# Optimization experiments

Hardware: AMD Instinct MI355X
Metric: run time of the kernel (lower is better)

The kernel has to match this reference:

```python
import jax, jax.numpy as jnp
import numpy as np

EMBED_DIM = 1024
NUM_HEADS = 16
DEPTH = EMBED_DIM // NUM_HEADS
SCALE_FACTOR = 0.5
SEQ = 2048
BATCH = 2


def setup_inputs() -> dict:
    key = jax.random.key(0)
    ks = jax.random.split(key, 6)
    x = jax.random.normal(ks[0], (SEQ, BATCH, EMBED_DIM), dtype=jnp.float32)
    attn_mask = jnp.zeros((SEQ, SEQ), dtype=jnp.float32)
    key_padding_mask = jnp.zeros((BATCH, SEQ), dtype=bool)
    # Linear params (torch convention: y = x @ W.T + b)
    s_in = 1.0 / np.sqrt(EMBED_DIM)
    qkv_w = jax.random.uniform(ks[1], (3 * EMBED_DIM, EMBED_DIM), jnp.float32, -s_in, s_in)
    qkv_b = jax.random.uniform(ks[2], (3 * EMBED_DIM,), jnp.float32, -s_in, s_in)
    out_w = jax.random.uniform(ks[3], (EMBED_DIM, EMBED_DIM), jnp.float32, -s_in, s_in)
    out_b = jax.random.uniform(ks[4], (EMBED_DIM,), jnp.float32, -s_in, s_in)
    return {"x": x, "attn_mask": attn_mask, "key_padding_mask": key_padding_mask,
            "qkv_w": qkv_w, "qkv_b": qkv_b, "out_w": out_w, "out_b": out_b}


def reference(x, attn_mask, key_padding_mask, qkv_w, qkv_b, out_w, out_b):
    # x: [S, B, E] -> [B, S, E]
    xb = jnp.transpose(x, (1, 0, 2))
    B, S, E = xb.shape
    qkv = xb @ qkv_w.T + qkv_b                       # [B, S, 3E]
    q, k, v = jnp.split(qkv, 3, axis=2)
    def split_heads(t):                              # [B, S, E] -> [B, H, S, d]
        return jnp.transpose(t.reshape(B, S, NUM_HEADS, DEPTH), (0, 2, 1, 3))
    q, k, v = split_heads(q), split_heads(k), split_heads(v)
    scores = jnp.einsum('bhqd,bhkd->bhqk', q, k) / (DEPTH ** SCALE_FACTOR)
    scores = jnp.where(key_padding_mask[:, None, None, :], -jnp.inf, scores)
    scores = scores + attn_mask[None, None, :, :]
    attn = jax.nn.softmax(scores, axis=-1)           # [B, H, S, S] (dropout p=0)
    wa = jnp.einsum('bhqk,bhkd->bhqd', attn, v)      # [B, H, S, d]
    wa = jnp.transpose(wa, (0, 2, 1, 3)).reshape(B, S, E)
    out = wa @ out_w.T + out_b                       # [B, S, E]
    out = jnp.transpose(out, (1, 0, 2))              # [S, B, E]
    attn_mean = jnp.mean(attn, axis=1)               # [B, S, S]
    return out, attn_mean
```

## Files before the change

kernel.cpp:

```cpp
#include <hip/hip_runtime.h>
#include <hip/hip_bf16.h>


#define Sq 2048
#define Bb 2
#define Ee 1024
#define Hh 16
#define Dd 64
#define LOG2E 1.4426950408889634f
#define QSCALE 0.18033688011112042f

typedef __attribute__((ext_vector_type(8))) short bhalf8;
typedef __attribute__((ext_vector_type(4))) float f32x4;

__device__ __forceinline__ void gld16(const __hip_bfloat16* g, __hip_bfloat16* l) {
    __builtin_amdgcn_global_load_lds(
        (const __attribute__((address_space(1))) unsigned int*)g,
        (__attribute__((address_space(3))) unsigned int*)l, 16, 0, 0);
}

__device__ __forceinline__ int pkbf(float a, float b) {
    union { __hip_bfloat16 h[2]; int i; } u;
    u.h[0] = __float2bfloat16(a);
    u.h[1] = __float2bfloat16(b);
    return u.i;
}

__device__ __forceinline__ int tile_off(int s) {
    return ((s >> 2) & 1) * 2048 + (s >> 7) * 512 + (s & 3) * 128 + ((s >> 3) & 15) * 8;
}

__device__ __forceinline__ int kperm(int p) {
    return (p & 3) | (((p >> 5) & 1) << 2) | ((p & 12) << 1) | (((p >> 4) & 1) << 5);
}

__global__ __launch_bounds__(256) void prep_k(
    const float* __restrict__ x, const float* __restrict__ am,
    const unsigned int* __restrict__ kpm32,
    const float* __restrict__ qkv_w, const float* __restrict__ out_w,
    __hip_bfloat16* __restrict__ xb, __hip_bfloat16* __restrict__ qwb,
    __hip_bfloat16* __restrict__ owb, unsigned int* __restrict__ flag)
{
    const long i = (long)blockIdx.x*256 + threadIdx.x;
    if (i < 1048576) {
        float4 v = ((const float4*)am)[i];
        bool nz = (v.x != 0.f) | (v.y != 0.f) | (v.z != 0.f) | (v.w != 0.f);
        if (i < 1024) nz |= (kpm32[i] != 0u);
        if (__ballot(nz)) { if ((threadIdx.x & 63) == 0) atomicOr(flag, 1u); }
    } else if (i < 2097152) {
        const long j = i - 1048576;
        const int m = (int)(j >> 8), e4 = (int)(j & 255);
        const int b = m >> 11, s = m & 2047;
        float4 v = ((const float4*)x)[(size_t)(s*Bb + b)*256 + e4];
        union { __hip_bfloat16 h[4]; uint2 u; } o;
        o.h[0]=__float2bfloat16(v.x); o.h[1]=__float2bfloat16(v.y);
        o.h[2]=__float2bfloat16(v.z); o.h[3]=__float2bfloat16(v.w);
        ((uint2*)xb)[(size_t)m*256 + e4] = o.u;
    } else if (i < 2883584) {
        const long j = i - 2097152;
        float4 v = ((const float4*)qkv_w)[j];
        union { __hip_bfloat16 h[4]; uint2 u; } o;
        o.h[0]=__float2bfloat16(v.x); o.h[1]=__float2bfloat16(v.y);
        o.h[2]=__float2bfloat16(v.z); o.h[3]=__float2bfloat16(v.w);
        ((uint2*)qwb)[j] = o.u;
    } else if (i < 3145728) {
        const long j = i - 2883584;
        float4 v = ((const float4*)out_w)[j];
        union { __hip_bfloat16 h[4]; uint2 u; } o;
        o.h[0]=__float2bfloat16(v.x); o.h[1]=__float2bfloat16(v.y);
        o.h[2]=__float2bfloat16(v.z); o.h[3]=__float2bfloat16(v.w);
        ((uint2*)owb)[j] = o.u;
    }
}

__global__ __launch_bounds__(256) void gemm_qkv(
    const __hip_bfloat16* __restrict__ A, const __hip_bfloat16* __restrict__ Bw,
    const float* __restrict__ bias,
    __hip_bfloat16* __restrict__ Qp, __hip_bfloat16* __restrict__ Kp,
    __hip_bfloat16* __restrict__ Vt)
{
    __shared__ __align__(16) __hip_bfloat16 As[128*32];
    __shared__ __align__(16) __hip_bfloat16 Bs[128*32];
    const int t = threadIdx.x;
    const int l = t & 63, lm = l & 15, quad = l >> 4;
    const int w = t >> 6;
    const int mw = (w & 1)*64, nw = (w >> 1)*64;
    const int m0 = blockIdx.y*128, n0 = blockIdx.x*128;

    const int srow = t >> 2;
    const int scol = (t & 3)*8;
    const __hip_bfloat16* ag = A  + (size_t)(m0 + srow)*1024 + scol;
    const __hip_bfloat16* bg = Bw + (size_t)(n0 + srow)*1024 + scol;
    __hip_bfloat16* al = As + t*8;
    __hip_bfloat16* bl = Bs + t*8;

    f32x4 acc[4][4] = {};
    for (int k0 = 0; k0 < 1024; k0 += 32) {
        __syncthreads();
        gld16(ag + k0, al);
        gld16(ag + (size_t)64*1024 + k0, al + 2048);
        gld16(bg + k0, bl);
        gld16(bg + (size_t)64*1024 + k0, bl + 2048);
        __syncthreads();
        bhalf8 af[4], bf[4];
#pragma unroll
        for (int i = 0; i < 4; i++) {
            af[i] = *(const bhalf8*)&As[(mw + i*16 + lm)*32 + quad*8];
            bf[i] = *(const bhalf8*)&Bs[(nw + i*16 + lm)*32 + quad*8];
        }
#pragma unroll
        for (int mf = 0; mf < 4; mf++)
#pragma unroll
            for (int nf = 0; nf < 4; nf++)
                acc[mf][nf] = __builtin_amdgcn_mfma_f32_16x16x32_bf16(af[mf], bf[nf], acc[mf][nf], 0,0,0);
    }
#pragma unroll
    for (int nf = 0; nf < 4; nf++) {
        const int n = n0 + nw + nf*16 + lm;
        const float bz = bias[n];
        const int which = n >> 10, hh = (n >> 6) & 15, dd = n & 63;
#pragma unroll
        for (int mf = 0; mf < 4; mf++)
#pragma unroll
            for (int r = 0; r < 4; r++) {
                const int m = m0 + mw + mf*16 + quad*4 + r;
                const int b2 = m >> 11, s2 = m & 2047;
                const float vf = acc[mf][nf][r] + bz;
                if (which == 0)
                    Qp[((size_t)(b2*Hh + hh)*Sq + s2)*Dd + dd] = __float2bfloat16(vf * QSCALE);
                else if (which == 1)
                    Kp[((size_t)(b2*Hh + hh)*Sq + s2)*Dd + dd] = __float2bfloat16(vf);
                else
                    Vt[((size_t)(b2*Hh + hh)*Dd + dd)*Sq + s2] = __float2bfloat16(vf);
            }
    }
}

__global__ __launch_bounds__(256, 4) void attn_mfma(
    const __hip_bfloat16* __restrict__ Qp, const __hip_bfloat16* __restrict__ Kp,
    const __hip_bfloat16* __restrict__ Vt,
    const float* __restrict__ am, const unsigned char* __restrict__ kpm,
    const unsigned int* __restrict__ flag,
    __hip_bfloat16* __restrict__ wa, float* __restrict__ rlbuf)
{
    __shared__ __align__(16) __hip_bfloat16 Ks[4096];
    __shared__ __align__(16) __hip_bfloat16 Vs[4096];
    const int t = threadIdx.x;
    const int w = t >> 6, l = t & 63, lm = l & 15, quad = l >> 4;
    const int blk = blockIdx.x;
    const int xcd = blk & 7;
    const int qt  = (blk >> 3) & 31;
    const int grp = blk >> 8;
    const int bh  = grp*8 + xcd;
    const int b   = bh >> 4, h = bh & 15;
    const int q   = qt*64 + w*16 + lm;
    const bool masked = (flag[0] != 0u);

    const __hip_bfloat16* qbase = Qp + (size_t)bh*Sq*Dd;
    const __hip_bfloat16* kbase = Kp + (size_t)bh*Sq*Dd;
    const __hip_bfloat16* vbase = Vt + (size_t)bh*Dd*Sq;

    bhalf8 bq[2];
    bq[0] = *(const bhalf8*)(qbase + (size_t)q*Dd + quad*8);
    bq[1] = *(const bhalf8*)(qbase + (size_t)q*Dd + quad*8 + 32);

    f32x4 o[4] = {};
    float lsum = 0.f;

    const int off0 = tile_off(t), off1 = tile_off(t + 256);
    const int krow0 = kperm(t >> 3);
    const int krow1 = kperm(32 + (t >> 3));
    const int kcol  = (t & 7)*8;

    uint4 kreg0 = *(const uint4*)(kbase + (size_t)krow0*Dd + kcol);
    uint4 kreg1 = *(const uint4*)(kbase + (size_t)krow1*Dd + kcol);
    uint4 vreg0 = *(const uint4*)(vbase + (size_t)(t >> 3)*Sq + (t & 7)*8);
    uint4 vreg1 = *(const uint4*)(vbase + (size_t)((t + 256) >> 3)*Sq + (t & 7)*8);

    for (int kt = 0; kt < 32; kt++) {
        __syncthreads();
        *(uint4*)&Ks[off0] = kreg0;
        *(uint4*)&Ks[off1] = kreg1;
        *(uint4*)&Vs[off0] = vreg0;
        *(uint4*)&Vs[off1] = vreg1;
        if (kt < 31) {
            const int kn = (kt + 1)*64;
            kreg0 = *(const uint4*)(kbase + (size_t)(kn + krow0)*Dd + kcol);
            kreg1 = *(const uint4*)(kbase + (size_t)(kn + krow1)*Dd + kcol);
            vreg0 = *(const uint4*)(vbase + (size_t)(t >> 3)*Sq + kn + (t & 7)*8);
            vreg1 = *(const uint4*)(vbase + (size_t)((t + 256) >> 3)*Sq + kn + (t & 7)*8);
        }
        __syncthreads();

        const int k0 = kt*64;
        f32x4 s[4] = {};
#pragma unroll
        for (int f = 0; f < 2; f++) {
            bhalf8 ak[4];
#pragma unroll
            for (int j = 0; j < 4; j++)
                ak[j] = *(const bhalf8*)&Ks[f*2048 + j*512 + l*8];
#pragma unroll
            for (int j = 0; j < 4; j++)
                s[j] = __builtin_amdgcn_mfma_f32_16x16x32_bf16(ak[j], bq[f], s[j], 0,0,0);
        }

        int pk[4][2];
#pragma unroll
        for (int j = 0; j < 4; j++) {
            float p[4];
#pragma unroll
            for (int r = 0; r < 4; r++) {
                float sv = s[j][r];
                if (masked) {
                    const int key = k0 + 32*(j & 1) + 8*quad + 4*(j >> 1) + r;
                    const float km = kpm[b*Sq + key] ? -1e30f : 0.0f;
                    sv += (am[(size_t)q*Sq + key] + km) * LOG2E;
                }
                p[r] = exp2f(sv);
            }
            lsum += (p[0]+p[1]) + (p[2]+p[3]);
            pk[j][0] = pkbf(p[0], p[1]);
            pk[j][1] = pkbf(p[2], p[3]);
        }

#pragma unroll
        for (int ks = 0; ks < 2; ks++) {
            union { int i[4]; bhalf8 v; } bp;
            bp.i[0] = pk[ks][0];
            bp.i[1] = pk[ks][1];
            bp.i[2] = pk[ks + 2][0];
            bp.i[3] = pk[ks + 2][1];
            bhalf8 av[4];
#pragma unroll
            for (int nd = 0; nd < 4; nd++)
                av[nd] = *(const bhalf8*)&Vs[ks*2048 + nd*512 + l*8];
#pragma unroll
            for (int nd = 0; nd < 4; nd++)
                o[nd] = __builtin_amdgcn_mfma_f32_16x16x32_bf16(av[nd], bp.v, o[nd], 0,0,0);
        }
    }

    lsum += __shfl_xor(lsum, 16, 64);
    lsum += __shfl_xor(lsum, 32, 64);
    const float rl = 1.0f / lsum;
    if (quad == 0) rlbuf[(size_t)bh*Sq + q] = rl;

#pragma unroll
    for (int nd = 0; nd < 4; nd++) {
        union { __hip_bfloat16 hx[4]; uint2 u; } ou;
#pragma unroll
        for (int r = 0; r < 4; r++) ou.hx[r] = __float2bfloat16(o[nd][r] * rl);
        *(uint2*)(wa + ((size_t)b*Sq + q)*Ee + h*Dd + nd*16 + quad*4) = ou.u;
    }
}

__global__ __launch_bounds__(256, 4) void attn_mean_k(
    const __hip_bfloat16* __restrict__ Qp, const __hip_bfloat16* __restrict__ Kp,
    const float* __restrict__ am, const unsigned char* __restrict__ kpm,
    const unsigned int* __restrict__ flag,
    const float* __restrict__ rlbuf, float* __restrict__ attn_mean)
{
    __shared__ __align__(16) __hip_bfloat16 Ks[4096];
    __shared__ __align__(16) __hip_bfloat16 Qs[8192];
    const int t = threadIdx.x;
    const int w = t >> 6, l = t & 63, lm = l & 15, quad = l >> 4;
    const int b  = blockIdx.z;
    const int q0 = blockIdx.y * 128;
    const int kc = blockIdx.x * 64;
    const int q0w = q0 + w*32;
    const bool masked = (flag[0] != 0u);

    const int koff = tile_off(t);
    const int koff1 = tile_off(t + 256);
    int qoff[4];
#pragma unroll
    for (int i = 0; i < 4; i++) {
        const int s = t + i*256;
        qoff[i] = (s >> 8)*2048 + ((s >> 7) & 1)*1024 + ((s >> 2) & 1)*512
                + (s & 3)*128 + ((s >> 3) & 15)*8;
    }

    float macc[2][4][4] = {};

    const __hip_bfloat16* kb0 = Kp + ((size_t)(b*Hh)*Sq + kc)*Dd;
    const __hip_bfloat16* qb0 = Qp + ((size_t)(b*Hh)*Sq + q0)*Dd;
    uint4 kr0 = *(const uint4*)(kb0 + (size_t)t*8);
    uint4 kr1 = *(const uint4*)(kb0 + (size_t)(t + 256)*8);
    uint4 qr[4];
#pragma unroll
    for (int i = 0; i < 4; i++) qr[i] = *(const uint4*)(qb0 + (size_t)(t + i*256)*8);

    for (int h = 0; h < Hh; h++) {
        __syncthreads();
        *(uint4*)&Ks[koff]  = kr0;
        *(uint4*)&Ks[koff1] = kr1;
#pragma unroll
        for (int i = 0; i < 4; i++) *(uint4*)&Qs[qoff[i]] = qr[i];
        if (h < Hh-1) {
            const __hip_bfloat16* kbn = Kp + ((size_t)(b*Hh + h+1)*Sq + kc)*Dd;
            const __hip_bfloat16* qbn = Qp + ((size_t)(b*Hh + h+1)*Sq + q0)*Dd;
            kr0 = *(const uint4*)(kbn + (size_t)t*8);
            kr1 = *(const uint4*)(kbn + (size_t)(t + 256)*8);
#pragma unroll
            for (int i = 0; i < 4; i++) qr[i] = *(const uint4*)(qbn + (size_t)(t + i*256)*8);
        }
        __syncthreads();

        const int bh = b*Hh + h;
        bhalf8 bk[8];
#pragma unroll
        for (int f = 0; f < 2; f++)
#pragma unroll
            for (int j = 0; j < 4; j++)
                bk[f*4+j] = *(const bhalf8*)&Ks[f*2048 + j*512 + l*8];

#pragma unroll
        for (int su = 0; su < 2; su++) {
            f32x4 s[4] = {};
#pragma unroll
            for (int f = 0; f < 2; f++) {
                bhalf8 aq = *(const bhalf8*)&Qs[w*2048 + su*1024 + f*512 + l*8];
#pragma unroll
                for (int j = 0; j < 4; j++)
                    s[j] = __builtin_amdgcn_mfma_f32_16x16x32_bf16(aq, bk[f*4+j], s[j], 0,0,0);
            }
            float rl4[4];
#pragma unroll
            for (int r = 0; r < 4; r++)
                rl4[r] = rlbuf[(size_t)bh*Sq + q0w + su*16 + quad*4 + r] * 0.0625f;
#pragma unroll
            for (int j = 0; j < 4; j++)
#pragma unroll
                for (int r = 0; r < 4; r++) {
                    float sv = s[j][r];
                    if (masked) {
                        const int key = kc + j*16 + lm;
                        const float km = kpm[b*Sq + key] ? -1e30f : 0.0f;
                        sv += (am[(size_t)(q0w + su*16 + quad*4 + r)*Sq + key] + km) * LOG2E;
                    }
                    macc[su][j][r] += exp2f(sv) * rl4[r];
                }
        }
    }
#pragma unroll
    for (int su = 0; su < 2; su++)
#pragma unroll
        for (int j = 0; j < 4; j++)
#pragma unroll
            for (int r = 0; r < 4; r++)
                attn_mean[((size_t)b*Sq + q0w + su*16 + quad*4 + r)*Sq + kc + j*16 + lm] =
                    macc[su][j][r];
}

__global__ __launch_bounds__(256) void gemm_out(
    const __hip_bfloat16* __restrict__ A, const __hip_bfloat16* __restrict__ Bw,
    const float* __restrict__ bias, float* __restrict__ outp)
{
    __shared__ __align__(16) __hip_bfloat16 As[128*32];
    __shared__ __align__(16) __hip_bfloat16 Bs[128*32];
    const int t = threadIdx.x;
    const int l = t & 63, lm = l & 15, quad = l >> 4;
    const int w = t >> 6;
    const int mw = (w & 1)*64, nw = (w >> 1)*64;
    const int m0 = blockIdx.y*128, n0 = blockIdx.x*128;

    const int srow = t >> 2;
    const int scol = (t & 3)*8;
    const __hip_bfloat16* ag = A  + (size_t)(m0 + srow)*1024 + scol;
    const __hip_bfloat16* bg = Bw + (size_t)(n0 + srow)*1024 + scol;
    __hip_bfloat16* al = As + t*8;
    __hip_bfloat16* bl = Bs + t*8;

    f32x4 acc[4][4] = {};
    for (int k0 = 0; k0 < 1024; k0 += 32) {
        __syncthreads();
        gld16(ag + k0, al);
        gld16(ag + (size_t)64*1024 + k0, al + 2048);
        gld16(bg + k0, bl);
        gld16(bg + (size_t)64*1024 + k0, bl + 2048);
        __syncthreads();
        bhalf8 af[4], bf[4];
#pragma unroll
        for (int i = 0; i < 4; i++) {
            af[i] = *(const bhalf8*)&As[(mw + i*16 + lm)*32 + quad*8];
            bf[i] = *(const bhalf8*)&Bs[(nw + i*16 + lm)*32 + quad*8];
        }
#pragma unroll
        for (int mf = 0; mf < 4; mf++)
#pragma unroll
            for (int nf = 0; nf < 4; nf++)
                acc[mf][nf] = __builtin_amdgcn_mfma_f32_16x16x32_bf16(af[mf], bf[nf], acc[mf][nf], 0,0,0);
    }
#pragma unroll
    for (int nf = 0; nf < 4; nf++) {
        const int n = n0 + nw + nf*16 + lm;
        const float bz = bias[n];
#pragma unroll
        for (int mf = 0; mf < 4; mf++)
#pragma unroll
            for (int r = 0; r < 4; r++) {
                const int m = m0 + mw + mf*16 + quad*4 + r;
                const int b2 = m >> 11, s2 = m & 2047;
                outp[((size_t)s2*Bb + b2)*Ee + n] = acc[mf][nf][r] + bz;
            }
    }
}

extern "C" void kernel_launch(void* const* d_in, const int* in_sizes, int n_in,
                              void* d_out, int out_size, void* d_ws, size_t ws_size,
                              hipStream_t stream) {
    const float*         x         = (const float*)d_in[0];
    const float*         attn_mask = (const float*)d_in[1];
    const unsigned char* kpm       = (const unsigned char*)d_in[2];
    const float*         qkv_w     = (const float*)d_in[3];
    const float*         qkv_b     = (const float*)d_in[4];
    const float*         out_w     = (const float*)d_in[5];
    const float*         out_b     = (const float*)d_in[6];

    float* outp      = (float*)d_out;
    float* attn_mean = outp + 4194304;

    __hip_bfloat16* xb  = (__hip_bfloat16*)d_ws;
    __hip_bfloat16* qwb = xb  + 4194304;
    __hip_bfloat16* owb = qwb + 3145728;
    __hip_bfloat16* Qp  = owb + 1048576;
    __hip_bfloat16* Kp  = Qp  + 4194304;
    __hip_bfloat16* Vt  = Kp  + 4194304;
    __hip_bfloat16* wab = Vt  + 4194304;
    float* rlbuf        = (float*)(wab + 4194304);
    unsigned int* flag  = (unsigned int*)(rlbuf + 65536);

    hipMemsetAsync(flag, 0, sizeof(unsigned int), stream);
    prep_k<<<12288, 256, 0, stream>>>(x, attn_mask, (const unsigned int*)kpm,
                                      qkv_w, out_w, xb, qwb, owb, flag);
    gemm_qkv<<<dim3(24, 32), 256, 0, stream>>>(xb, qwb, qkv_b, Qp, Kp, Vt);
    attn_mfma<<<dim3(1024), 256, 0, stream>>>(Qp, Kp, Vt, attn_mask, kpm, flag, wab, rlbuf);
    attn_mean_k<<<dim3(32, 16, Bb), 256, 0, stream>>>(Qp, Kp, attn_mask, kpm, flag, rlbuf, attn_mean);
    gemm_out<<<dim3(8, 32), 256, 0, stream>>>(wab, owb, out_b, outp);
}
```

Measured before the change: 370.2 us.

## Halve attn_mean query tile and load Q/K via direct global-to-LDS copies

The attention-mean kernel now handles 64 queries per block instead of 128, doubling the grid to 2048 blocks and halving the Q shared-memory tile. The register-staged prefetch of the next head's Q/K tiles is replaced by global_load_lds direct copies issued each head iteration. K fragments are now read from LDS inside the MFMA loop instead of being cached in registers. The goal is higher occupancy and less register pressure, at the cost of losing explicit prefetch overlap and re-reading each K tile for twice as many query blocks.

```diff
diff --git a/kernel.cpp b/kernel.cpp
--- a/kernel.cpp
+++ b/kernel.cpp
@@ -262,95 +262,61 @@
     const float* __restrict__ rlbuf, float* __restrict__ attn_mean)
 {
     __shared__ __align__(16) __hip_bfloat16 Ks[4096];
-    __shared__ __align__(16) __hip_bfloat16 Qs[8192];
+    __shared__ __align__(16) __hip_bfloat16 Qs[4096];
     const int t = threadIdx.x;
     const int w = t >> 6, l = t & 63, lm = l & 15, quad = l >> 4;
     const int b  = blockIdx.z;
-    const int q0 = blockIdx.y * 128;
+    const int q0 = blockIdx.y * 64;
     const int kc = blockIdx.x * 64;
-    const int q0w = q0 + w*32;
     const bool masked = (flag[0] != 0u);
 
-    const int koff = tile_off(t);
-    const int koff1 = tile_off(t + 256);
-    int qoff[4];
-#pragma unroll
-    for (int i = 0; i < 4; i++) {
-        const int s = t + i*256;
-        qoff[i] = (s >> 8)*2048 + ((s >> 7) & 1)*1024 + ((s >> 2) & 1)*512
-                + (s & 3)*128 + ((s >> 3) & 15)*8;
-    }
-
-    float macc[2][4][4] = {};
-
-    const __hip_bfloat16* kb0 = Kp + ((size_t)(b*Hh)*Sq + kc)*Dd;
-    const __hip_bfloat16* qb0 = Qp + ((size_t)(b*Hh)*Sq + q0)*Dd;
-    uint4 kr0 = *(const uint4*)(kb0 + (size_t)t*8);
-    uint4 kr1 = *(const uint4*)(kb0 + (size_t)(t + 256)*8);
-    uint4 qr[4];
-#pragma unroll
-    for (int i = 0; i < 4; i++) qr[i] = *(const uint4*)(qb0 + (size_t)(t + i*256)*8);
+    const int s0 = ((w & 1) << 8) | (lm << 3) | ((w >> 1) << 2) | (l >> 4);
+    __hip_bfloat16* kl = Ks + w*1024;
+    __hip_bfloat16* ql = Qs + w*1024;
+
+    float macc[4][4] = {};
+    const float* rlp = rlbuf + (size_t)(b*Hh)*Sq + q0 + w*16 + quad*4;
 
     for (int h = 0; h < Hh; h++) {
-        __syncthreads();
-        *(uint4*)&Ks[koff]  = kr0;
-        *(uint4*)&Ks[koff1] = kr1;
-#pragma unroll
-        for (int i = 0; i < 4; i++) *(uint4*)&Qs[qoff[i]] = qr[i];
-        if (h < Hh-1) {
-            const __hip_bfloat16* kbn = Kp + ((size_t)(b*Hh + h+1)*Sq + kc)*Dd;
-            const __hip_bfloat16* qbn = Qp + ((size_t)(b*Hh + h+1)*Sq + q0)*Dd;
-            kr0 = *(const uint4*)(kbn + (size_t)t*8);
-            kr1 = *(const uint4*)(kbn + (size_t)(t + 256)*8);
-#pragma unroll
-            for (int i = 0; i < 4; i++) qr[i] = *(const uint4*)(qbn + (size_t)(t + i*256)*8);
-        }
-        __syncthreads();
-
-        const int bh = b*Hh + h;
-        bhalf8 bk[8];
-#pragma unroll
-        for (int f = 0; f < 2; f++)
-#pragma unroll
-            for (int j = 0; j < 4; j++)
-                bk[f*4+j] = *(const bhalf8*)&Ks[f*2048 + j*512 + l*8];
-
-#pragma unroll
-        for (int su = 0; su < 2; su++) {
-            f32x4 s[4] = {};
-#pragma unroll
-            for (int f = 0; f < 2; f++) {
-                bhalf8 aq = *(const bhalf8*)&Qs[w*2048 + su*1024 + f*512 + l*8];
-#pragma unroll
-                for (int j = 0; j < 4; j++)
-                    s[j] = __builtin_amdgcn_mfma_f32_16x16x32_bf16(aq, bk[f*4+j], s[j], 0,0,0);
+        const __hip_bfloat16* kg = Kp + ((size_t)(b*Hh + h)*Sq + kc)*Dd + s0*8;
+        const __hip_bfloat16* qg = Qp + ((size_t)(b*Hh + h)*Sq + q0)*Dd + s0*8;
+        __syncthreads();
+        gld16(kg, kl);       gld16(kg + 1024, kl + 512);
+        gld16(qg, ql);       gld16(qg + 1024, ql + 512);
+        __syncthreads();
+
+        f32x4 s[4] = {};
+#pragma unroll
+        for (int f = 0; f < 2; f++) {
+            bhalf8 aq = *(const bhalf8*)&Qs[f*2048 + w*512 + l*8];
+#pragma unroll
+            for (int j = 0; j < 4; j++) {
+                bhalf8 bk = *(const bhalf8*)&Ks[f*2048 + j*512 + l*8];
+                s[j] = __builtin_amdgcn_mfma_f32_16x16x32_bf16(aq, bk, s[j], 0,0,0);
             }
-            float rl4[4];
-#pragma unroll
-            for (int r = 0; r < 4; r++)
-                rl4[r] = rlbuf[(size_t)bh*Sq + q0w + su*16 + quad*4 + r] * 0.0625f;
-#pragma unroll
-            for (int j = 0; j < 4; j++)
-#pragma unroll
-                for (int r = 0; r < 4; r++) {
-                    float sv = s[j][r];
-                    if (masked) {
-                        const int key = kc + j*16 + lm;
-                        const float km = kpm[b*Sq + key] ? -1e30f : 0.0f;
-                        sv += (am[(size_t)(q0w + su*16 + quad*4 + r)*Sq + key] + km) * LOG2E;
-                    }
-                    macc[su][j][r] += exp2f(sv) * rl4[r];
+        }
+        float rl4[4];
+#pragma unroll
+        for (int r = 0; r < 4; r++) rl4[r] = rlp[(size_t)h*Sq + r] * 0.0625f;
+#pragma unroll
+        for (int j = 0; j < 4; j++)
+#pragma unroll
+            for (int r = 0; r < 4; r++) {
+                float sv = s[j][r];
+                if (masked) {
+                    const int key = kc + j*16 + lm;
+                    const float km = kpm[b*Sq + key] ? -1e30f : 0.0f;
+                    sv += (am[(size_t)(q0 + w*16 + quad*4 + r)*Sq + key] + km) * LOG2E;
                 }
-        }
-    }
-#pragma unroll
-    for (int su = 0; su < 2; su++)
-#pragma unroll
-        for (int j = 0; j < 4; j++)
-#pragma unroll
-            for (int r = 0; r < 4; r++)
-                attn_mean[((size_t)b*Sq + q0w + su*16 + quad*4 + r)*Sq + kc + j*16 + lm] =
-                    macc[su][j][r];
+                macc[j][r] += exp2f(sv) * rl4[r];
+            }
+    }
+#pragma unroll
+    for (int j = 0; j < 4; j++)
+#pragma unroll
+        for (int r = 0; r < 4; r++)
+            attn_mean[((size_t)b*Sq + q0 + w*16 + quad*4 + r)*Sq + kc + j*16 + lm] =
+                macc[j][r];
 }
 
 __global__ __launch_bounds__(256) void gemm_out(
@@ -436,6 +402,6 @@
                                       qkv_w, out_w, xb, qwb, owb, flag);
     gemm_qkv<<<dim3(24, 32), 256, 0, stream>>>(xb, qwb, qkv_b, Qp, Kp, Vt);
     attn_mfma<<<dim3(1024), 256, 0, stream>>>(Qp, Kp, Vt, attn_mask, kpm, flag, wab, rlbuf);
-    attn_mean_k<<<dim3(32, 16, Bb), 256, 0, stream>>>(Qp, Kp, attn_mask, kpm, flag, rlbuf, attn_mean);
+    attn_mean_k<<<dim3(32, 32, Bb), 256, 0, stream>>>(Qp, Kp, attn_mask, kpm, flag, rlbuf, attn_mean);
     gemm_out<<<dim3(8, 32), 256, 0, stream>>>(wab, owb, out_b, outp);
 }
```

New measurement: 654.5 us. 1.77x slower.
